# Performance work log

Measured on AMD Instinct MI355X. Metric: run time of the kernel, lower is better.

## Reference

```python
import jax, jax.numpy as jnp
import numpy as np

EPS = 1e-12
ALPHA = 0.5


def mlp(x, W1, b1, W2, b2):
    # 2-layer MLP (dropout inactive in eval mode) + row-wise l2 norm * 10
    h = jax.nn.relu(x @ W1 + b1)
    y = h @ W2 + b2
    n = jnp.maximum(jnp.linalg.norm(y, axis=-1, keepdims=True), EPS)
    return y / n * 10.0


def setup_inputs() -> dict:
    key = jax.random.key(0)
    ks = jax.random.split(key, 12)
    T, N, F = 3, 100000, 128
    M, E = 4, 65536
    B, H, O = 65536, 128, 64
    X = jax.random.normal(ks[0], (T, N, F), dtype=jnp.float32)
    s_features = jax.random.normal(ks[1], (B, F), dtype=jnp.float32)
    features_map = jax.random.randint(ks[2], (T, N), 0, N)
    s_idxs = jax.random.randint(ks[3], (M, T, E), 0, B)
    t_idxs = jax.random.randint(ks[4], (M, T, E), 0, N)
    weightss = jax.random.uniform(ks[5], (M, T, E), dtype=jnp.float32)
    W1 = jax.random.normal(ks[6], (F, H), dtype=jnp.float32) / np.sqrt(F)
    b1 = jnp.zeros((H,), dtype=jnp.float32)
    W2 = jax.random.normal(ks[7], (H, O), dtype=jnp.float32) / np.sqrt(H)
    b2 = jnp.zeros((O,), dtype=jnp.float32)
    metapath_weights = jnp.ones((M,), dtype=jnp.float32)
    ntype_weights = jnp.ones((T,), dtype=jnp.float32)
    return {"X": X, "s_features": s_features, "features_map": features_map,
            "s_idxs": s_idxs, "t_idxs": t_idxs, "weightss": weightss,
            "batch_size": B, "W1": W1, "b1": b1, "W2": W2, "b2": b2,
            "metapath_weights": metapath_weights, "ntype_weights": ntype_weights}


def reference(X, s_features, features_map, s_idxs, t_idxs, weightss,
              batch_size, W1, b1, W2, b2, metapath_weights, ntype_weights):
    M, T, E = s_idxs.shape
    O = W2.shape[1]
    nm = jax.nn.softmax(metapath_weights)  # [M]
    nt = jax.nn.softmax(ntype_weights)     # [T]
    t_arr = jnp.arange(T)[None, :, None]   # [1,T,1]
    map_idx = features_map[t_arr, t_idxs]  # [M,T,E]
    feats = X[t_arr, map_idx]              # [M,T,E,F] gather
    y = mlp(feats, W1, b1, W2, b2)         # [M,T,E,O]
    # fold metapath & type weights into per-edge weights (scatter is linear)
    ew = weightss * nt[None, :, None] * nm[:, None, None]  # [M,T,E]
    contrib = (y * ew[..., None]).reshape(-1, O)
    seg = s_idxs.reshape(-1)
    out = jax.ops.segment_sum(contrib, seg, num_segments=batch_size)  # [B,O]
    out = (1.0 - ALPHA) * out + ALPHA * mlp(s_features, W1, b1, W2, b2)
    return jax.nn.log_softmax(out, axis=1)
```

## Files before the change

kernel.cpp:

```cpp
#include <hip/hip_runtime.h>

#define Fdim 128
#define Hdim 128
#define Odim 64
#define RT 64
#define ECAP 64
#define EPSV 1e-12f
#define ALPHAV 0.5f

typedef _Float16 h8_t __attribute__((ext_vector_type(8)));
typedef _Float16 h4_t __attribute__((ext_vector_type(4)));
typedef float f32x4 __attribute__((ext_vector_type(4)));

#define W2T_OFF 0
#define X0_OFF  16384
#define H0_OFF  49152
#define LDS_BYTES 81920
#define WIMG_BYTES 49152

extern "C" __global__ __launch_bounds__(512, 4)
void mlp_all(const float* __restrict__ X, const float* __restrict__ S,
             const char* __restrict__ wimg, const float* __restrict__ b1,
             const float* __restrict__ b2,
             _Float16* __restrict__ Yh, float* __restrict__ out,
             int TN, int rows_total, int ngroups)
{
    extern __shared__ char smem[];
    const int tid  = threadIdx.x;
    const int wave = tid >> 6;
    const int lane = tid & 63;
    const int c = lane & 15;
    const int g = lane >> 4;

    #pragma unroll
    for (int i = 0; i < 2; ++i) {
        int idx = tid + i * 512;
        float4 v = *(const float4*)(wimg + 32768 + idx * 16);
        *(float4*)(smem + W2T_OFF + idx * 16) = v;
    }

    h8_t w1f[4];
    {
        int r0 = wave * 16 + c;
        #pragma unroll
        for (int kt = 0; kt < 4; ++kt)
            w1f[kt] = *(const h8_t*)(wimg + (((r0 << 8) + (kt << 6) + (g << 4)) ^ ((c & 7) << 4)));
    }

    const int hbase = wave * 16 + 4 * g;
    float b1v[4];
    #pragma unroll
    for (int j = 0; j < 4; ++j) b1v[j] = b1[hbase + j];
    float bb[4];
    #pragma unroll
    for (int ct = 0; ct < 4; ++ct) bb[ct] = b2[ct * 16 + c];

    float4 pf[4];
    int grp = blockIdx.x;
    #pragma unroll
    for (int it = 0; it < 4; ++it) {
        int idx = tid + it * 512;
        int r = idx >> 5, c4 = idx & 31;
        int rowg = grp * RT + r;
        float4 v = make_float4(0.f, 0.f, 0.f, 0.f);
        if (rowg < TN)               v = *(const float4*)(X + (size_t)rowg * Fdim + c4 * 4);
        else if (rowg < rows_total)  v = *(const float4*)(S + (size_t)(rowg - TN) * Fdim + c4 * 4);
        pf[it] = v;
    }
    #pragma unroll
    for (int it = 0; it < 4; ++it) {
        int idx = tid + it * 512;
        int r = idx >> 5, c4 = idx & 31;
        h4_t hv;
        hv[0] = (_Float16)pf[it].x; hv[1] = (_Float16)pf[it].y;
        hv[2] = (_Float16)pf[it].z; hv[3] = (_Float16)pf[it].w;
        *(h4_t*)(smem + X0_OFF + ((r * 256 + c4 * 8) ^ ((r & 7) << 4))) = hv;
    }
    __syncthreads();

    int cur = 0;
    for (; grp < ngroups; grp += gridDim.x, cur ^= 1) {
        const int gnext = grp + gridDim.x;
        const int xb = X0_OFF + cur * 16384;
        const int hb = H0_OFF + cur * 16384;
        const int xn = X0_OFF + (cur ^ 1) * 16384;

        #pragma unroll
        for (int it = 0; it < 4; ++it) {
            int idx = tid + it * 512;
            int r = idx >> 5, c4 = idx & 31;
            int rowg = gnext * RT + r;
            float4 v = make_float4(0.f, 0.f, 0.f, 0.f);
            if (rowg < TN)               v = *(const float4*)(X + (size_t)rowg * Fdim + c4 * 4);
            else if (rowg < rows_total)  v = *(const float4*)(S + (size_t)(rowg - TN) * Fdim + c4 * 4);
            pf[it] = v;
        }

        f32x4 acc[4];
        #pragma unroll
        for (int r = 0; r < 4; ++r) acc[r] = (f32x4){0.f, 0.f, 0.f, 0.f};

        #pragma unroll
        for (int kt = 0; kt < 4; ++kt) {
            #pragma unroll
            for (int rt = 0; rt < 4; ++rt) {
                int xr = rt * 16 + c;
                h8_t bf = *(const h8_t*)(smem + xb + ((xr * 256 + kt * 64 + g * 16) ^ ((c & 7) << 4)));
                acc[rt] = __builtin_amdgcn_mfma_f32_16x16x32_f16(w1f[kt], bf, acc[rt], 0, 0, 0);
            }
        }

        #pragma unroll
        for (int rt = 0; rt < 4; ++rt) {
            int xr = rt * 16 + c;
            h4_t hv;
            #pragma unroll
            for (int j = 0; j < 4; ++j) {
                float hval = acc[rt][j] + b1v[j];
                hval = fmaxf(hval, 0.f);
                hv[j] = (_Float16)hval;
            }
            *(h4_t*)(smem + hb + ((xr * 256 + hbase * 2) ^ ((xr & 7) << 4))) = hv;
        }

        #pragma unroll
        for (int it = 0; it < 4; ++it) {
            int idx = tid + it * 512;
            int r = idx >> 5, c4 = idx & 31;
            h4_t hv;
            hv[0] = (_Float16)pf[it].x; hv[1] = (_Float16)pf[it].y;
            hv[2] = (_Float16)pf[it].z; hv[3] = (_Float16)pf[it].w;
            *(h4_t*)(smem + xn + ((r * 256 + c4 * 8) ^ ((r & 7) << 4))) = hv;
        }

        __syncthreads();

        if (wave < 4) {
            f32x4 acc2[4];
            #pragma unroll
            for (int ct = 0; ct < 4; ++ct) acc2[ct] = (f32x4){0.f, 0.f, 0.f, 0.f};

            #pragma unroll
            for (int kt = 0; kt < 4; ++kt) {
                int xr = wave * 16 + c;
                h8_t a = *(const h8_t*)(smem + hb + ((xr * 256 + kt * 64 + g * 16) ^ ((xr & 7) << 4)));
                #pragma unroll
                for (int ct = 0; ct < 4; ++ct) {
                    int wr = ct * 16 + c;
                    h8_t bf = *(const h8_t*)(smem + W2T_OFF + ((wr * 256 + kt * 64 + g * 16) ^ ((c & 7) << 4)));
                    acc2[ct] = __builtin_amdgcn_mfma_f32_16x16x32_f16(a, bf, acc2[ct], 0, 0, 0);
                }
            }

            float y[4][4];
            float ssq[4] = {0.f, 0.f, 0.f, 0.f};
            #pragma unroll
            for (int ct = 0; ct < 4; ++ct) {
                #pragma unroll
                for (int j = 0; j < 4; ++j) {
                    float v = acc2[ct][j] + bb[ct];
                    y[ct][j] = v;
                    ssq[j] += v * v;
                }
            }
            #pragma unroll
            for (int j = 0; j < 4; ++j) {
                float s = ssq[j];
                s += __shfl_xor(s, 1);
                s += __shfl_xor(s, 2);
                s += __shfl_xor(s, 4);
                s += __shfl_xor(s, 8);
                float n  = fmaxf(sqrtf(s), EPSV);
                float sc = 10.0f / n;
                int rowg = grp * RT + wave * 16 + 4 * g + j;
                if (rowg < TN) {
                    _Float16* dst = Yh + (size_t)rowg * Odim;
                    #pragma unroll
                    for (int ct = 0; ct < 4; ++ct)
                        dst[ct * 16 + c] = (_Float16)(y[ct][j] * sc);
                } else if (rowg < rows_total) {
                    float* dst = out + (size_t)(rowg - TN) * Odim;
                    #pragma unroll
                    for (int ct = 0; ct < 4; ++ct)
                        dst[ct * 16 + c] = ALPHAV * y[ct][j] * sc;
                }
            }
        }
    }
}

extern "C" __global__ __launch_bounds__(256)
void prep_all(const float* __restrict__ W1, const float* __restrict__ W2,
              char* __restrict__ wimg, int* __restrict__ cnt, int B)
{
    if (blockIdx.x < 96) {
        int idx = blockIdx.x * 256 + threadIdx.x;
        if (idx < 16384) {
            int h = idx >> 7, f = idx & 127;
            float v = W1[(size_t)f * Hdim + h];
            int byte = (h * 256 + f * 2) ^ ((h & 7) << 4);
            *(_Float16*)(wimg + byte) = (_Float16)v;
        } else if (idx < 24576) {
            int i2 = idx - 16384;
            int o = i2 >> 7, k = i2 & 127;
            float v = W2[(size_t)k * Odim + o];
            int byte = 32768 + ((o * 256 + k * 2) ^ ((o & 7) << 4));
            *(_Float16*)(wimg + byte) = (_Float16)v;
        }
    } else {
        int i = (blockIdx.x - 96) * 256 + threadIdx.x;
        if (i < B) cnt[i] = 0;
    }
}

extern "C" __global__ __launch_bounds__(256)
void scatter_edges(const int* __restrict__ s_idxs, const int* __restrict__ t_idxs,
                   const float* __restrict__ wss, const int* __restrict__ fmap,
                   const float* __restrict__ mw, const float* __restrict__ tw,
                   int* __restrict__ cnt, int2* __restrict__ edat,
                   int Nn, int Tt, int Mm, int Eslab)
{
    const int slab = blockIdx.y;
    const int t    = slab % Tt;
    const int tN   = t * Nn;
    float mmax = -1e30f, tmax = -1e30f, msum = 0.f, tsum = 0.f;
    for (int i = 0; i < Mm; ++i) mmax = fmaxf(mmax, mw[i]);
    for (int i = 0; i < Mm; ++i) msum += expf(mw[i] - mmax);
    for (int i = 0; i < Tt; ++i) tmax = fmaxf(tmax, tw[i]);
    for (int i = 0; i < Tt; ++i) tsum += expf(tw[i] - tmax);
    const float scale = (1.0f - ALPHAV) * expf(mw[slab / Tt] - mmax) * expf(tw[t] - tmax)
                        / (msum * tsum);

    int i = blockIdx.x * 256 + threadIdx.x;
    if (i >= Eslab) return;
    int e = slab * Eslab + i;
    int si   = s_idxs[e];
    int yrow = tN + fmap[tN + t_idxs[e]];
    float w  = wss[e] * scale;
    int pos = atomicAdd(cnt + si, 1);
    if (pos < ECAP)
        edat[(size_t)si * ECAP + pos] = make_int2(yrow, __float_as_int(w));
}

extern "C" __global__ __launch_bounds__(256)
void row_gather(const int2* __restrict__ edgedat, const int* __restrict__ cnt,
                const _Float16* __restrict__ Yh, float* __restrict__ out, int B)
{
    const int lane = threadIdx.x & 63;
    const int grp8 = lane >> 3;
    const int sub  = lane & 7;
    int b = blockIdx.x * 4 + (threadIdx.x >> 6);
    if (b >= B) return;
    int n = cnt[b];
    if (n > ECAP) n = ECAP;
    const int2* ebase = edgedat + (size_t)b * ECAP;

    float acc[8];
    #pragma unroll
    for (int j = 0; j < 8; ++j) acc[j] = 0.f;

    for (int e = grp8; e < n; e += 8) {
        int2 ed = ebase[e];
        float w = __int_as_float(ed.y);
        h8_t y8 = *(const h8_t*)(Yh + (size_t)ed.x * Odim + sub * 8);
        #pragma unroll
        for (int j = 0; j < 8; ++j) acc[j] += w * (float)y8[j];
    }
    #pragma unroll
    for (int d = 8; d < 64; d <<= 1) {
        #pragma unroll
        for (int j = 0; j < 8; ++j) acc[j] += __shfl_xor(acc[j], d);
    }
    const float* orow = out + (size_t)b * Odim + sub * 8;
    float v[8];
    #pragma unroll
    for (int j = 0; j < 8; ++j) v[j] = orow[j] + acc[j];

    float mx = v[0];
    #pragma unroll
    for (int j = 1; j < 8; ++j) mx = fmaxf(mx, v[j]);
    #pragma unroll
    for (int d = 1; d < 8; d <<= 1) mx = fmaxf(mx, __shfl_xor(mx, d));
    float sm = 0.f;
    #pragma unroll
    for (int j = 0; j < 8; ++j) sm += expf(v[j] - mx);
    #pragma unroll
    for (int d = 1; d < 8; d <<= 1) sm += __shfl_xor(sm, d);
    float lg = mx + logf(sm);

    if (grp8 == 0) {
        float* dst = out + (size_t)b * Odim + sub * 8;
        #pragma unroll
        for (int j = 0; j < 8; ++j) dst[j] = v[j] - lg;
    }
}


extern "C" __global__ __launch_bounds__(256)
void edge_scatter(const int* __restrict__ s_idxs, const int* __restrict__ t_idxs,
                  const float* __restrict__ weightss, const int* __restrict__ fmap,
                  const _Float16* __restrict__ Yh, const float* __restrict__ mw,
                  const float* __restrict__ tw,
                  float* __restrict__ out, int Nn, int Tt, int Mm, int Eslab)
{
    const int lane = threadIdx.x & 63;
    const int slab = blockIdx.y;
    const int t    = slab % Tt;
    const int tN   = t * Nn;
    float mmax = -1e30f, tmax = -1e30f, msum = 0.f, tsum = 0.f;
    for (int i = 0; i < Mm; ++i) mmax = fmaxf(mmax, mw[i]);
    for (int i = 0; i < Mm; ++i) msum += expf(mw[i] - mmax);
    for (int i = 0; i < Tt; ++i) tmax = fmaxf(tmax, tw[i]);
    for (int i = 0; i < Tt; ++i) tsum += expf(tw[i] - tmax);
    const float scale = (1.0f - ALPHAV) * expf(mw[slab / Tt] - mmax) * expf(tw[t] - tmax)
                        / (msum * tsum);

    const int wid  = blockIdx.x * (blockDim.x >> 6) + (threadIdx.x >> 6);
    const int off  = wid * 64;
    if (off >= Eslab) return;

    const int ebase = slab * Eslab + off;
    int   e_ok = (off + lane) < Eslab;
    int   eidx = ebase + (e_ok ? lane : 0);
    int   si   = s_idxs[eidx];
    int   ti   = t_idxs[eidx];
    float w    = e_ok ? (weightss[eidx] * scale) : 0.0f;
    int   yrow = tN + fmap[tN + ti];

    #pragma unroll 8
    for (int i = 0; i < 64; ++i) {
        int   nd = __builtin_amdgcn_readlane(yrow, i);
        int   s  = __builtin_amdgcn_readlane(si, i);
        float ws = __uint_as_float(__builtin_amdgcn_readlane(__float_as_uint(w), i));
        float yv = (float)Yh[(size_t)nd * Odim + lane];
        atomicAdd(out + (size_t)s * Odim + lane, yv * ws);
    }
}

extern "C" __global__ __launch_bounds__(256)
void log_softmax_rows(float* __restrict__ out, int Brows)
{
    int lane = threadIdx.x & 63;
    int r = blockIdx.x * 4 + (threadIdx.x >> 6);
    if (r >= Brows) return;
    float* row = out + (size_t)r * Odim;
    float v = row[lane];
    float mx = v;
    for (int off = 32; off > 0; off >>= 1) mx = fmaxf(mx, __shfl_xor(mx, off));
    float ex = expf(v - mx);
    float s = ex;
    for (int off = 32; off > 0; off >>= 1) s += __shfl_xor(s, off);
    row[lane] = v - mx - logf(s);
}

extern "C" void kernel_launch(void* const* d_in, const int* in_sizes, int n_in,
                              void* d_out, int out_size, void* d_ws, size_t ws_size,
                              hipStream_t stream)
{
    const float* X   = (const float*)d_in[0];
    const float* S   = (const float*)d_in[1];
    const int*   fmap= (const int*)d_in[2];
    const int*   sidx= (const int*)d_in[3];
    const int*   tidx= (const int*)d_in[4];
    const float* wss = (const float*)d_in[5];
    const float* W1  = (const float*)d_in[7];
    const float* b1  = (const float*)d_in[8];
    const float* W2  = (const float*)d_in[9];
    const float* b2  = (const float*)d_in[10];
    const float* mw  = (const float*)d_in[11];
    const float* tw  = (const float*)d_in[12];
    float* out = (float*)d_out;

    const int M = in_sizes[11];
    const int T = in_sizes[12];
    const int H = in_sizes[8];
    const int Fv = in_sizes[7] / H;
    const int N = in_sizes[2] / T;
    const int nedges = in_sizes[3];
    const int E = nedges / (M * T);
    const int B = in_sizes[1] / Fv;
    const int TN = T * N;
    const int rows_total = TN + B;
    const int ngroups = (rows_total + RT - 1) / RT;

    char* wp = (char*)d_ws;
    size_t used = 0;
    auto alloc = [&](size_t bytes) -> char* {
        char* p = wp + used;
        used = (used + bytes + 255) & ~(size_t)255;
        return p;
    };
    _Float16* Yh   = (_Float16*)alloc((size_t)TN * Odim * sizeof(_Float16));
    char*     wimg = (char*)    alloc((size_t)WIMG_BYTES);
    int*      cntp = (int*)     alloc((size_t)B * sizeof(int));
    int2*     edat = (int2*)    alloc((size_t)B * ECAP * sizeof(int2));
    bool bucket_ok = used <= ws_size;

    hipFuncSetAttribute((const void*)mlp_all,
                        hipFuncAttributeMaxDynamicSharedMemorySize, LDS_BYTES);

    const int zb = (B + 255) / 256;
    prep_all<<<96 + zb, 256, 0, stream>>>(W1, W2, wimg, cntp, B);

    if (bucket_ok) {
        dim3 sg((E + 255) / 256, M * T);
        scatter_edges<<<sg, 256, 0, stream>>>(sidx, tidx, wss, fmap, mw, tw,
                                              cntp, edat, N, T, M, E);
        mlp_all<<<512, 512, LDS_BYTES, stream>>>(X, S, wimg, b1, b2, Yh, out,
                                                 TN, rows_total, ngroups);
        row_gather<<<(B + 3) / 4, 256, 0, stream>>>(edat, cntp, Yh, out, B);
    } else {
        mlp_all<<<512, 512, LDS_BYTES, stream>>>(X, S, wimg, b1, b2, Yh, out,
                                                 TN, rows_total, ngroups);
        int waves_per_slab = (E + 63) / 64;
        dim3 sg((waves_per_slab + 3) / 4, M * T);
        edge_scatter<<<sg, 256, 0, stream>>>(sidx, tidx, wss, fmap, Yh, mw, tw, out,
                                             N, T, M, E);
        log_softmax_rows<<<(B + 3) / 4, 256, 0, stream>>>(out, B);
    }
}
```

Before: 146.1 us.

## Warp-specialize MLP kernel into producer layer-1 and consumer layer-2 waves

Splits the 8 waves into 4 producer waves, which prefetch X rows and compute layer 1 across two H tiles each, and 4 consumer waves, which compute layer 2 for the previous group with W2 held in registers. The two layers of successive row groups overlap, and only one barrier per iteration remains. Because W2 no longer lives in LDS, the LDS footprint shrinks. The cost is higher register pressure (w2f array, doubled accumulators, 8 prefetch float4s) under launch bounds of 512 threads × 4 blocks, plus an extra epilogue pass.

```diff
diff --git a/kernel.cpp b/kernel.cpp
--- a/kernel.cpp
+++ b/kernel.cpp
@@ -12,10 +12,9 @@
 typedef _Float16 h4_t __attribute__((ext_vector_type(4)));
 typedef float f32x4 __attribute__((ext_vector_type(4)));
 
-#define W2T_OFF 0
-#define X0_OFF  16384
-#define H0_OFF  49152
-#define LDS_BYTES 81920
+#define X0_OFF  0
+#define H0_OFF  32768
+#define LDS_BYTES 65536
 #define WIMG_BYTES 49152
 
 extern "C" __global__ __launch_bounds__(512, 4)
@@ -31,111 +30,126 @@
     const int lane = tid & 63;
     const int c = lane & 15;
     const int g = lane >> 4;
-
-    #pragma unroll
-    for (int i = 0; i < 2; ++i) {
-        int idx = tid + i * 512;
-        float4 v = *(const float4*)(wimg + 32768 + idx * 16);
-        *(float4*)(smem + W2T_OFF + idx * 16) = v;
-    }
-
-    h8_t w1f[4];
-    {
-        int r0 = wave * 16 + c;
-        #pragma unroll
-        for (int kt = 0; kt < 4; ++kt)
-            w1f[kt] = *(const h8_t*)(wimg + (((r0 << 8) + (kt << 6) + (g << 4)) ^ ((c & 7) << 4)));
-    }
-
-    const int hbase = wave * 16 + 4 * g;
-    float b1v[4];
-    #pragma unroll
-    for (int j = 0; j < 4; ++j) b1v[j] = b1[hbase + j];
+    const bool producer = wave >= 4;
+    const int pw = wave - 4;
+    const int ptid = tid & 255;
+
+    h8_t w1f[2][4];
+    float b1v[2][4];
+    h8_t w2f[4][4];
     float bb[4];
-    #pragma unroll
-    for (int ct = 0; ct < 4; ++ct) bb[ct] = b2[ct * 16 + c];
-
-    float4 pf[4];
+
+    if (producer) {
+        #pragma unroll
+        for (int ht = 0; ht < 2; ++ht) {
+            int r0 = pw * 32 + ht * 16 + c;
+            #pragma unroll
+            for (int kt = 0; kt < 4; ++kt)
+                w1f[ht][kt] = *(const h8_t*)(wimg + (((r0 << 8) + (kt << 6) + (g << 4)) ^ ((c & 7) << 4)));
+            int hb2 = pw * 32 + ht * 16 + 4 * g;
+            #pragma unroll
+            for (int j = 0; j < 4; ++j) b1v[ht][j] = b1[hb2 + j];
+        }
+    } else {
+        #pragma unroll
+        for (int ct = 0; ct < 4; ++ct) {
+            int wr = ct * 16 + c;
+            #pragma unroll
+            for (int kt = 0; kt < 4; ++kt)
+                w2f[ct][kt] = *(const h8_t*)(wimg + 32768 + (((wr << 8) + (kt << 6) + (g << 4)) ^ ((c & 7) << 4)));
+            bb[ct] = b2[wr];
+        }
+    }
+
     int grp = blockIdx.x;
-    #pragma unroll
-    for (int it = 0; it < 4; ++it) {
-        int idx = tid + it * 512;
-        int r = idx >> 5, c4 = idx & 31;
-        int rowg = grp * RT + r;
-        float4 v = make_float4(0.f, 0.f, 0.f, 0.f);
-        if (rowg < TN)               v = *(const float4*)(X + (size_t)rowg * Fdim + c4 * 4);
-        else if (rowg < rows_total)  v = *(const float4*)(S + (size_t)(rowg - TN) * Fdim + c4 * 4);
-        pf[it] = v;
-    }
-    #pragma unroll
-    for (int it = 0; it < 4; ++it) {
-        int idx = tid + it * 512;
-        int r = idx >> 5, c4 = idx & 31;
-        h4_t hv;
-        hv[0] = (_Float16)pf[it].x; hv[1] = (_Float16)pf[it].y;
-        hv[2] = (_Float16)pf[it].z; hv[3] = (_Float16)pf[it].w;
-        *(h4_t*)(smem + X0_OFF + ((r * 256 + c4 * 8) ^ ((r & 7) << 4))) = hv;
-    }
-    __syncthreads();
-
-    int cur = 0;
-    for (; grp < ngroups; grp += gridDim.x, cur ^= 1) {
-        const int gnext = grp + gridDim.x;
-        const int xb = X0_OFF + cur * 16384;
-        const int hb = H0_OFF + cur * 16384;
-        const int xn = X0_OFF + (cur ^ 1) * 16384;
-
-        #pragma unroll
-        for (int it = 0; it < 4; ++it) {
-            int idx = tid + it * 512;
+    float4 pf[8];
+    if (producer) {
+        #pragma unroll
+        for (int it = 0; it < 8; ++it) {
+            int idx = ptid + it * 256;
             int r = idx >> 5, c4 = idx & 31;
-            int rowg = gnext * RT + r;
+            int rowg = grp * RT + r;
             float4 v = make_float4(0.f, 0.f, 0.f, 0.f);
             if (rowg < TN)               v = *(const float4*)(X + (size_t)rowg * Fdim + c4 * 4);
             else if (rowg < rows_total)  v = *(const float4*)(S + (size_t)(rowg - TN) * Fdim + c4 * 4);
             pf[it] = v;
         }
-
-        f32x4 acc[4];
-        #pragma unroll
-        for (int r = 0; r < 4; ++r) acc[r] = (f32x4){0.f, 0.f, 0.f, 0.f};
-
-        #pragma unroll
-        for (int kt = 0; kt < 4; ++kt) {
-            #pragma unroll
-            for (int rt = 0; rt < 4; ++rt) {
-                int xr = rt * 16 + c;
-                h8_t bf = *(const h8_t*)(smem + xb + ((xr * 256 + kt * 64 + g * 16) ^ ((c & 7) << 4)));
-                acc[rt] = __builtin_amdgcn_mfma_f32_16x16x32_f16(w1f[kt], bf, acc[rt], 0, 0, 0);
-            }
-        }
-
-        #pragma unroll
-        for (int rt = 0; rt < 4; ++rt) {
-            int xr = rt * 16 + c;
-            h4_t hv;
-            #pragma unroll
-            for (int j = 0; j < 4; ++j) {
-                float hval = acc[rt][j] + b1v[j];
-                hval = fmaxf(hval, 0.f);
-                hv[j] = (_Float16)hval;
-            }
-            *(h4_t*)(smem + hb + ((xr * 256 + hbase * 2) ^ ((xr & 7) << 4))) = hv;
-        }
-
-        #pragma unroll
-        for (int it = 0; it < 4; ++it) {
-            int idx = tid + it * 512;
+        #pragma unroll
+        for (int it = 0; it < 8; ++it) {
+            int idx = ptid + it * 256;
             int r = idx >> 5, c4 = idx & 31;
             h4_t hv;
             hv[0] = (_Float16)pf[it].x; hv[1] = (_Float16)pf[it].y;
             hv[2] = (_Float16)pf[it].z; hv[3] = (_Float16)pf[it].w;
-            *(h4_t*)(smem + xn + ((r * 256 + c4 * 8) ^ ((r & 7) << 4))) = hv;
-        }
-
-        __syncthreads();
-
-        if (wave < 4) {
+            *(h4_t*)(smem + X0_OFF + ((r * 256 + c4 * 8) ^ ((r & 7) << 4))) = hv;
+        }
+    }
+    __syncthreads();
+
+    int prev = -1;
+    int pbuf = 0;
+    for (; grp < ngroups; grp += gridDim.x, pbuf ^= 1) {
+        const int xb = X0_OFF + pbuf * 16384;
+        const int hb = H0_OFF + pbuf * 16384;
+
+        if (producer) {
+            const int gnext = grp + gridDim.x;
+            #pragma unroll
+            for (int it = 0; it < 8; ++it) {
+                int idx = ptid + it * 256;
+                int r = idx >> 5, c4 = idx & 31;
+                int rowg = gnext * RT + r;
+                float4 v = make_float4(0.f, 0.f, 0.f, 0.f);
+                if (rowg < TN)               v = *(const float4*)(X + (size_t)rowg * Fdim + c4 * 4);
+                else if (rowg < rows_total)  v = *(const float4*)(S + (size_t)(rowg - TN) * Fdim + c4 * 4);
+                pf[it] = v;
+            }
+
+            f32x4 acc[2][4];
+            #pragma unroll
+            for (int ht = 0; ht < 2; ++ht)
+                #pragma unroll
+                for (int rt = 0; rt < 4; ++rt) acc[ht][rt] = (f32x4){0.f, 0.f, 0.f, 0.f};
+
+            #pragma unroll
+            for (int kt = 0; kt < 4; ++kt) {
+                #pragma unroll
+                for (int rt = 0; rt < 4; ++rt) {
+                    int xr = rt * 16 + c;
+                    h8_t bf = *(const h8_t*)(smem + xb + ((xr * 256 + kt * 64 + g * 16) ^ ((c & 7) << 4)));
+                    acc[0][rt] = __builtin_amdgcn_mfma_f32_16x16x32_f16(w1f[0][kt], bf, acc[0][rt], 0, 0, 0);
+                    acc[1][rt] = __builtin_amdgcn_mfma_f32_16x16x32_f16(w1f[1][kt], bf, acc[1][rt], 0, 0, 0);
+                }
+            }
+
+            #pragma unroll
+            for (int ht = 0; ht < 2; ++ht) {
+                int hb2 = pw * 32 + ht * 16 + 4 * g;
+                #pragma unroll
+                for (int rt = 0; rt < 4; ++rt) {
+                    int xr = rt * 16 + c;
+                    h4_t hv;
+                    #pragma unroll
+                    for (int j = 0; j < 4; ++j) {
+                        float hval = acc[ht][rt][j] + b1v[ht][j];
+                        hval = fmaxf(hval, 0.f);
+                        hv[j] = (_Float16)hval;
+                    }
+                    *(h4_t*)(smem + hb + ((xr * 256 + hb2 * 2) ^ ((xr & 7) << 4))) = hv;
+                }
+            }
+
+            #pragma unroll
+            for (int it = 0; it < 8; ++it) {
+                int idx = ptid + it * 256;
+                int r = idx >> 5, c4 = idx & 31;
+                h4_t hv;
+                hv[0] = (_Float16)pf[it].x; hv[1] = (_Float16)pf[it].y;
+                hv[2] = (_Float16)pf[it].z; hv[3] = (_Float16)pf[it].w;
+                *(h4_t*)(smem + (xb ^ 16384) + ((r * 256 + c4 * 8) ^ ((r & 7) << 4))) = hv;
+            }
+        } else if (prev >= 0) {
+            const int hprev = H0_OFF + (pbuf ^ 1) * 16384;
             f32x4 acc2[4];
             #pragma unroll
             for (int ct = 0; ct < 4; ++ct) acc2[ct] = (f32x4){0.f, 0.f, 0.f, 0.f};
@@ -143,13 +157,10 @@
             #pragma unroll
             for (int kt = 0; kt < 4; ++kt) {
                 int xr = wave * 16 + c;
-                h8_t a = *(const h8_t*)(smem + hb + ((xr * 256 + kt * 64 + g * 16) ^ ((xr & 7) << 4)));
-                #pragma unroll
-                for (int ct = 0; ct < 4; ++ct) {
-                    int wr = ct * 16 + c;
-                    h8_t bf = *(const h8_t*)(smem + W2T_OFF + ((wr * 256 + kt * 64 + g * 16) ^ ((c & 7) << 4)));
-                    acc2[ct] = __builtin_amdgcn_mfma_f32_16x16x32_f16(a, bf, acc2[ct], 0, 0, 0);
-                }
+                h8_t a = *(const h8_t*)(smem + hprev + ((xr * 256 + kt * 64 + g * 16) ^ ((xr & 7) << 4)));
+                #pragma unroll
+                for (int ct = 0; ct < 4; ++ct)
+                    acc2[ct] = __builtin_amdgcn_mfma_f32_16x16x32_f16(a, w2f[ct][kt], acc2[ct], 0, 0, 0);
             }
 
             float y[4][4];
@@ -172,7 +183,7 @@
                 s += __shfl_xor(s, 8);
                 float n  = fmaxf(sqrtf(s), EPSV);
                 float sc = 10.0f / n;
-                int rowg = grp * RT + wave * 16 + 4 * g + j;
+                int rowg = prev * RT + wave * 16 + 4 * g + j;
                 if (rowg < TN) {
                     _Float16* dst = Yh + (size_t)rowg * Odim;
                     #pragma unroll
@@ -184,6 +195,59 @@
                     for (int ct = 0; ct < 4; ++ct)
                         dst[ct * 16 + c] = ALPHAV * y[ct][j] * sc;
                 }
+            }
+        }
+
+        prev = grp;
+        __syncthreads();
+    }
+
+    if (!producer && prev >= 0) {
+        const int hprev = H0_OFF + (pbuf ^ 1) * 16384;
+        f32x4 acc2[4];
+        #pragma unroll
+        for (int ct = 0; ct < 4; ++ct) acc2[ct] = (f32x4){0.f, 0.f, 0.f, 0.f};
+
+        #pragma unroll
+        for (int kt = 0; kt < 4; ++kt) {
+            int xr = wave * 16 + c;
+            h8_t a = *(const h8_t*)(smem + hprev + ((xr * 256 + kt * 64 + g * 16) ^ ((xr & 7) << 4)));
+            #pragma unroll
+            for (int ct = 0; ct < 4; ++ct)
+                acc2[ct] = __builtin_amdgcn_mfma_f32_16x16x32_f16(a, w2f[ct][kt], acc2[ct], 0, 0, 0);
+        }
+
+        float y[4][4];
+        float ssq[4] = {0.f, 0.f, 0.f, 0.f};
+        #pragma unroll
+        for (int ct = 0; ct < 4; ++ct) {
+            #pragma unroll
+            for (int j = 0; j < 4; ++j) {
+                float v = acc2[ct][j] + bb[ct];
+                y[ct][j] = v;
+                ssq[j] += v * v;
+            }
+        }
+        #pragma unroll
+        for (int j = 0; j < 4; ++j) {
+            float s = ssq[j];
+            s += __shfl_xor(s, 1);
+            s += __shfl_xor(s, 2);
+            s += __shfl_xor(s, 4);
+            s += __shfl_xor(s, 8);
+            float n  = fmaxf(sqrtf(s), EPSV);
+            float sc = 10.0f / n;
+            int rowg = prev * RT + wave * 16 + 4 * g + j;
+            if (rowg < TN) {
+                _Float16* dst = Yh + (size_t)rowg * Odim;
+                #pragma unroll
+                for (int ct = 0; ct < 4; ++ct)
+                    dst[ct * 16 + c] = (_Float16)(y[ct][j] * sc);
+            } else if (rowg < rows_total) {
+                float* dst = out + (size_t)(rowg - TN) * Odim;
+                #pragma unroll
+                for (int ct = 0; ct < 4; ++ct)
+                    dst[ct * 16 + c] = ALPHAV * y[ct][j] * sc;
             }
         }
     }
```

Result: slower. 294.2 us (+101.4%).

## Replace persistent double-buffered MLP kernel with one-tile-per-block launch

Applied to the files above, without the earlier changes.

Drops the persistent grid-stride loop with its register prefetch and double-buffered LDS. Each block now processes a single 64-row tile, and the grid is sized to the number of tiles. W1 and W2 are pre-packed in the MFMA fragment order, so lanes load them straight from global memory with contiguous 16-byte reads. W2 is no longer staged in LDS, which cuts LDS to 32 KB and removes the dynamic shared-memory attribute call, aiming for higher occupancy and less per-block setup. The cost is losing explicit load/compute overlap and re-reading the weights from global or L2 in every block.

```diff
diff --git a/kernel.cpp b/kernel.cpp
--- a/kernel.cpp
+++ b/kernel.cpp
@@ -12,10 +12,9 @@
 typedef _Float16 h4_t __attribute__((ext_vector_type(4)));
 typedef float f32x4 __attribute__((ext_vector_type(4)));
 
-#define W2T_OFF 0
-#define X0_OFF  16384
-#define H0_OFF  49152
-#define LDS_BYTES 81920
+#define X_OFF   0
+#define H_OFF   16384
+#define LDS_BYTES 32768
 #define WIMG_BYTES 49152
 
 extern "C" __global__ __launch_bounds__(512, 4)
@@ -23,7 +22,7 @@
              const char* __restrict__ wimg, const float* __restrict__ b1,
              const float* __restrict__ b2,
              _Float16* __restrict__ Yh, float* __restrict__ out,
-             int TN, int rows_total, int ngroups)
+             int TN, int rows_total)
 {
     extern __shared__ char smem[];
     const int tid  = threadIdx.x;
@@ -31,159 +30,112 @@
     const int lane = tid & 63;
     const int c = lane & 15;
     const int g = lane >> 4;
-
-    #pragma unroll
-    for (int i = 0; i < 2; ++i) {
-        int idx = tid + i * 512;
-        float4 v = *(const float4*)(wimg + 32768 + idx * 16);
-        *(float4*)(smem + W2T_OFF + idx * 16) = v;
-    }
+    const int row0 = blockIdx.x * RT;
 
     h8_t w1f[4];
-    {
-        int r0 = wave * 16 + c;
-        #pragma unroll
-        for (int kt = 0; kt < 4; ++kt)
-            w1f[kt] = *(const h8_t*)(wimg + (((r0 << 8) + (kt << 6) + (g << 4)) ^ ((c & 7) << 4)));
-    }
+    #pragma unroll
+    for (int kt = 0; kt < 4; ++kt)
+        w1f[kt] = *(const h8_t*)(wimg + (((wave * 4 + kt) * 64 + lane) << 4));
 
     const int hbase = wave * 16 + 4 * g;
     float b1v[4];
     #pragma unroll
     for (int j = 0; j < 4; ++j) b1v[j] = b1[hbase + j];
-    float bb[4];
-    #pragma unroll
-    for (int ct = 0; ct < 4; ++ct) bb[ct] = b2[ct * 16 + c];
-
-    float4 pf[4];
-    int grp = blockIdx.x;
+
     #pragma unroll
     for (int it = 0; it < 4; ++it) {
         int idx = tid + it * 512;
         int r = idx >> 5, c4 = idx & 31;
-        int rowg = grp * RT + r;
+        int rowg = row0 + r;
         float4 v = make_float4(0.f, 0.f, 0.f, 0.f);
         if (rowg < TN)               v = *(const float4*)(X + (size_t)rowg * Fdim + c4 * 4);
         else if (rowg < rows_total)  v = *(const float4*)(S + (size_t)(rowg - TN) * Fdim + c4 * 4);
-        pf[it] = v;
-    }
-    #pragma unroll
-    for (int it = 0; it < 4; ++it) {
-        int idx = tid + it * 512;
-        int r = idx >> 5, c4 = idx & 31;
         h4_t hv;
-        hv[0] = (_Float16)pf[it].x; hv[1] = (_Float16)pf[it].y;
-        hv[2] = (_Float16)pf[it].z; hv[3] = (_Float16)pf[it].w;
-        *(h4_t*)(smem + X0_OFF + ((r * 256 + c4 * 8) ^ ((r & 7) << 4))) = hv;
+        hv[0] = (_Float16)v.x; hv[1] = (_Float16)v.y;
+        hv[2] = (_Float16)v.z; hv[3] = (_Float16)v.w;
+        *(h4_t*)(smem + X_OFF + ((r * 256 + c4 * 8) ^ ((r & 7) << 4))) = hv;
     }
     __syncthreads();
 
-    int cur = 0;
-    for (; grp < ngroups; grp += gridDim.x, cur ^= 1) {
-        const int gnext = grp + gridDim.x;
-        const int xb = X0_OFF + cur * 16384;
-        const int hb = H0_OFF + cur * 16384;
-        const int xn = X0_OFF + (cur ^ 1) * 16384;
-
-        #pragma unroll
-        for (int it = 0; it < 4; ++it) {
-            int idx = tid + it * 512;
-            int r = idx >> 5, c4 = idx & 31;
-            int rowg = gnext * RT + r;
-            float4 v = make_float4(0.f, 0.f, 0.f, 0.f);
-            if (rowg < TN)               v = *(const float4*)(X + (size_t)rowg * Fdim + c4 * 4);
-            else if (rowg < rows_total)  v = *(const float4*)(S + (size_t)(rowg - TN) * Fdim + c4 * 4);
-            pf[it] = v;
-        }
-
-        f32x4 acc[4];
-        #pragma unroll
-        for (int r = 0; r < 4; ++r) acc[r] = (f32x4){0.f, 0.f, 0.f, 0.f};
-
-        #pragma unroll
-        for (int kt = 0; kt < 4; ++kt) {
-            #pragma unroll
-            for (int rt = 0; rt < 4; ++rt) {
-                int xr = rt * 16 + c;
-                h8_t bf = *(const h8_t*)(smem + xb + ((xr * 256 + kt * 64 + g * 16) ^ ((c & 7) << 4)));
-                acc[rt] = __builtin_amdgcn_mfma_f32_16x16x32_f16(w1f[kt], bf, acc[rt], 0, 0, 0);
-            }
-        }
-
+    f32x4 acc[4];
+    #pragma unroll
+    for (int r = 0; r < 4; ++r) acc[r] = (f32x4){0.f, 0.f, 0.f, 0.f};
+
+    #pragma unroll
+    for (int kt = 0; kt < 4; ++kt) {
         #pragma unroll
         for (int rt = 0; rt < 4; ++rt) {
             int xr = rt * 16 + c;
-            h4_t hv;
+            h8_t bf = *(const h8_t*)(smem + X_OFF + ((xr * 256 + kt * 64 + g * 16) ^ ((c & 7) << 4)));
+            acc[rt] = __builtin_amdgcn_mfma_f32_16x16x32_f16(w1f[kt], bf, acc[rt], 0, 0, 0);
+        }
+    }
+
+    #pragma unroll
+    for (int rt = 0; rt < 4; ++rt) {
+        int xr = rt * 16 + c;
+        h4_t hv;
+        #pragma unroll
+        for (int j = 0; j < 4; ++j) {
+            float hval = acc[rt][j] + b1v[j];
+            hval = fmaxf(hval, 0.f);
+            hv[j] = (_Float16)hval;
+        }
+        *(h4_t*)(smem + H_OFF + ((xr * 256 + hbase * 2) ^ ((xr & 7) << 4))) = hv;
+    }
+    __syncthreads();
+
+    if (wave < 4) {
+        f32x4 acc2[4];
+        #pragma unroll
+        for (int ct = 0; ct < 4; ++ct) acc2[ct] = (f32x4){0.f, 0.f, 0.f, 0.f};
+
+        #pragma unroll
+        for (int kt = 0; kt < 4; ++kt) {
+            int xr = wave * 16 + c;
+            h8_t a = *(const h8_t*)(smem + H_OFF + ((xr * 256 + kt * 64 + g * 16) ^ ((xr & 7) << 4)));
+            #pragma unroll
+            for (int ct = 0; ct < 4; ++ct) {
+                h8_t bf = *(const h8_t*)(wimg + 32768 + (((ct * 4 + kt) * 64 + lane) << 4));
+                acc2[ct] = __builtin_amdgcn_mfma_f32_16x16x32_f16(a, bf, acc2[ct], 0, 0, 0);
+            }
+        }
+
+        float bb[4];
+        #pragma unroll
+        for (int ct = 0; ct < 4; ++ct) bb[ct] = b2[ct * 16 + c];
+
+        float y[4][4];
+        float ssq[4] = {0.f, 0.f, 0.f, 0.f};
+        #pragma unroll
+        for (int ct = 0; ct < 4; ++ct) {
             #pragma unroll
             for (int j = 0; j < 4; ++j) {
-                float hval = acc[rt][j] + b1v[j];
-                hval = fmaxf(hval, 0.f);
-                hv[j] = (_Float16)hval;
+                float v = acc2[ct][j] + bb[ct];
+                y[ct][j] = v;
+                ssq[j] += v * v;
             }
-            *(h4_t*)(smem + hb + ((xr * 256 + hbase * 2) ^ ((xr & 7) << 4))) = hv;
-        }
-
-        #pragma unroll
-        for (int it = 0; it < 4; ++it) {
-            int idx = tid + it * 512;
-            int r = idx >> 5, c4 = idx & 31;
-            h4_t hv;
-            hv[0] = (_Float16)pf[it].x; hv[1] = (_Float16)pf[it].y;
-            hv[2] = (_Float16)pf[it].z; hv[3] = (_Float16)pf[it].w;
-            *(h4_t*)(smem + xn + ((r * 256 + c4 * 8) ^ ((r & 7) << 4))) = hv;
-        }
-
-        __syncthreads();
-
-        if (wave < 4) {
-            f32x4 acc2[4];
-            #pragma unroll
-            for (int ct = 0; ct < 4; ++ct) acc2[ct] = (f32x4){0.f, 0.f, 0.f, 0.f};
-
-            #pragma unroll
-            for (int kt = 0; kt < 4; ++kt) {
-                int xr = wave * 16 + c;
-                h8_t a = *(const h8_t*)(smem + hb + ((xr * 256 + kt * 64 + g * 16) ^ ((xr & 7) << 4)));
+        }
+        #pragma unroll
+        for (int j = 0; j < 4; ++j) {
+            float s = ssq[j];
+            s += __shfl_xor(s, 1);
+            s += __shfl_xor(s, 2);
+            s += __shfl_xor(s, 4);
+            s += __shfl_xor(s, 8);
+            float n  = fmaxf(sqrtf(s), EPSV);
+            float sc = 10.0f / n;
+            int rowg = row0 + wave * 16 + 4 * g + j;
+            if (rowg < TN) {
+                _Float16* dst = Yh + (size_t)rowg * Odim;
                 #pragma unroll
-                for (int ct = 0; ct < 4; ++ct) {
-                    int wr = ct * 16 + c;
-                    h8_t bf = *(const h8_t*)(smem + W2T_OFF + ((wr * 256 + kt * 64 + g * 16) ^ ((c & 7) << 4)));
-                    acc2[ct] = __builtin_amdgcn_mfma_f32_16x16x32_f16(a, bf, acc2[ct], 0, 0, 0);
-                }
-            }
-
-            float y[4][4];
-            float ssq[4] = {0.f, 0.f, 0.f, 0.f};
-            #pragma unroll
-            for (int ct = 0; ct < 4; ++ct) {
+                for (int ct = 0; ct < 4; ++ct)
+                    dst[ct * 16 + c] = (_Float16)(y[ct][j] * sc);
+            } else if (rowg < rows_total) {
+                float* dst = out + (size_t)(rowg - TN) * Odim;
                 #pragma unroll
-                for (int j = 0; j < 4; ++j) {
-                    float v = acc2[ct][j] + bb[ct];
-                    y[ct][j] = v;
-                    ssq[j] += v * v;
-                }
-            }
-            #pragma unroll
-            for (int j = 0; j < 4; ++j) {
-                float s = ssq[j];
-                s += __shfl_xor(s, 1);
-                s += __shfl_xor(s, 2);
-                s += __shfl_xor(s, 4);
-                s += __shfl_xor(s, 8);
-                float n  = fmaxf(sqrtf(s), EPSV);
-                float sc = 10.0f / n;
-                int rowg = grp * RT + wave * 16 + 4 * g + j;
-                if (rowg < TN) {
-                    _Float16* dst = Yh + (size_t)rowg * Odim;
-                    #pragma unroll
-                    for (int ct = 0; ct < 4; ++ct)
-                        dst[ct * 16 + c] = (_Float16)(y[ct][j] * sc);
-                } else if (rowg < rows_total) {
-                    float* dst = out + (size_t)(rowg - TN) * Odim;
-                    #pragma unroll
-                    for (int ct = 0; ct < 4; ++ct)
-                        dst[ct * 16 + c] = ALPHAV * y[ct][j] * sc;
-                }
+                for (int ct = 0; ct < 4; ++ct)
+                    dst[ct * 16 + c] = ALPHAV * y[ct][j] * sc;
             }
         }
     }
@@ -196,16 +148,14 @@
     if (blockIdx.x < 96) {
         int idx = blockIdx.x * 256 + threadIdx.x;
         if (idx < 16384) {
-            int h = idx >> 7, f = idx & 127;
-            float v = W1[(size_t)f * Hdim + h];
-            int byte = (h * 256 + f * 2) ^ ((h & 7) << 4);
-            *(_Float16*)(wimg + byte) = (_Float16)v;
+            int j = idx & 7, l = (idx >> 3) & 63, kt = (idx >> 9) & 3, w = idx >> 11;
+            float v = W1[(size_t)(kt * 32 + (l >> 4) * 8 + j) * Hdim + (w * 16 + (l & 15))];
+            ((_Float16*)wimg)[idx] = (_Float16)v;
         } else if (idx < 24576) {
-            int i2 = idx - 16384;
-            int o = i2 >> 7, k = i2 & 127;
-            float v = W2[(size_t)k * Odim + o];
-            int byte = 32768 + ((o * 256 + k * 2) ^ ((o & 7) << 4));
-            *(_Float16*)(wimg + byte) = (_Float16)v;
+            int e2 = idx - 16384;
+            int j = e2 & 7, l = (e2 >> 3) & 63, kt = (e2 >> 9) & 3, ct = e2 >> 11;
+            float v = W2[(size_t)(kt * 32 + (l >> 4) * 8 + j) * Odim + (ct * 16 + (l & 15))];
+            ((_Float16*)(wimg + 32768))[e2] = (_Float16)v;
         }
     } else {
         int i = (blockIdx.x - 96) * 256 + threadIdx.x;
@@ -396,9 +346,6 @@
     int2*     edat = (int2*)    alloc((size_t)B * ECAP * sizeof(int2));
     bool bucket_ok = used <= ws_size;
 
-    hipFuncSetAttribute((const void*)mlp_all,
-                        hipFuncAttributeMaxDynamicSharedMemorySize, LDS_BYTES);
-
     const int zb = (B + 255) / 256;
     prep_all<<<96 + zb, 256, 0, stream>>>(W1, W2, wimg, cntp, B);
 
@@ -406,12 +353,12 @@
         dim3 sg((E + 255) / 256, M * T);
         scatter_edges<<<sg, 256, 0, stream>>>(sidx, tidx, wss, fmap, mw, tw,
                                               cntp, edat, N, T, M, E);
-        mlp_all<<<512, 512, LDS_BYTES, stream>>>(X, S, wimg, b1, b2, Yh, out,
-                                                 TN, rows_total, ngroups);
+        mlp_all<<<ngroups, 512, LDS_BYTES, stream>>>(X, S, wimg, b1, b2, Yh, out,
+                                                     TN, rows_total);
         row_gather<<<(B + 3) / 4, 256, 0, stream>>>(edat, cntp, Yh, out, B);
     } else {
-        mlp_all<<<512, 512, LDS_BYTES, stream>>>(X, S, wimg, b1, b2, Yh, out,
-                                                 TN, rows_total, ngroups);
+        mlp_all<<<ngroups, 512, LDS_BYTES, stream>>>(X, S, wimg, b1, b2, Yh, out,
+                                                     TN, rows_total);
         int waves_per_slab = (E + 63) / 64;
         dim3 sg((waves_per_slab + 3) / 4, M * T);
         edge_scatter<<<sg, 256, 0, stream>>>(sidx, tidx, wss, fmap, Yh, mw, tw, out,
```

After: 148.1 us. About the same (+1.4%).
